# Kernel optimization log

Measured on AMD Instinct MI355X. Metric: run time of the kernel, lower is better.

The kernel has to match this reference:

```python
import jax, jax.numpy as jnp
import numpy as np

B, T, D = 2, 2048, 1024
DCD = 4096            # intermediate_dim
RET = 128             # expert_retrieval_dim (split into 2 halves of 64)
NEXP = 4096           # num experts (perfect square)
NKEYS = 64            # sqrt(NEXP)
H = 4                 # n_experts_heads
KPH = 8               # n_experts_per_head


def setup_inputs() -> dict:
    key = jax.random.key(0)
    ks = jax.random.split(key, 10)
    s = lambda k, shape, scale: jax.random.normal(k, shape, jnp.float32) * scale
    return {
        "hidden_states": jax.random.normal(ks[0], (B, T, D), jnp.float32),
        "Wg": s(ks[1], (D, DCD), 0.02), "bg": jnp.zeros((DCD,), jnp.float32),
        "Wu": s(ks[2], (D, DCD), 0.02), "bu": jnp.zeros((DCD,), jnp.float32),
        "Wd": s(ks[3], (DCD, D), 0.02), "bd": jnp.zeros((D,), jnp.float32),
        "Wq": s(ks[4], (D, RET * H), 0.02),          # queries proj (no bias)
        "keys": s(ks[5], (H, NKEYS, 2, RET // 2), 0.02),  # torch inits zeros; randn for a meaningful baseline
        "down_embed": s(ks[6], (NEXP, D), 0.02),
        "up_embed": s(ks[7], (NEXP, D), 0.02),
    }


def reference(hidden_states, Wg, bg, Wu, bu, Wd, bd, Wq, keys, down_embed, up_embed):
    b, t, d = hidden_states.shape
    # product-key retrieval: split query into two halves (p=2)
    q = (hidden_states @ Wq).reshape(b, t, 2, H, RET // 2)
    sim = jnp.einsum('btphn,hkpn->pbthk', q, keys)          # [2,b,t,H,NKEYS]
    sc, ix = jax.lax.top_k(sim, KPH)                        # per-half top-k
    sx, sy = sc[0], sc[1]
    ixx, ixy = ix[0], ix[1]
    all_sc = (sx[..., :, None] + sy[..., None, :]).reshape(b, t, H, KPH * KPH)
    all_ix = (ixx[..., :, None] * NKEYS + ixy[..., None, :]).reshape(b, t, H, KPH * KPH)
    scores, pk = jax.lax.top_k(all_sc, KPH)                 # [b,t,H,KPH]
    idx = jnp.take_along_axis(all_ix, pk, axis=-1)          # expert ids
    de = down_embed[idx]                                    # [b,t,H,KPH,D] gather
    ue = up_embed[idx]                                      # [b,t,H,KPH,D] gather
    w = jnp.einsum('btd,bthkd->bthk', hidden_states, de)
    w = jax.nn.silu(w) * jax.nn.softmax(scores, axis=-1)
    experts_states = jnp.einsum('bthk,bthkd->btd', w, ue)
    mlp = (jax.nn.silu(hidden_states @ Wg + bg) * (hidden_states @ Wu + bu)) @ Wd + bd
    return mlp + experts_states
```

## Files before the change

kernel.cpp:

```cpp
#include <hip/hip_runtime.h>
#include <hip/hip_bf16.h>
#include <stdint.h>

typedef unsigned short u16;
typedef __attribute__((ext_vector_type(8))) short short8;
typedef __attribute__((ext_vector_type(4))) float f32x4;
typedef __attribute__((ext_vector_type(2))) float f32x2;

union B8 { short8 v; u16 u[8]; };
union U4 { unsigned long long q; u16 u[4]; };

__device__ __forceinline__ float b2f(u16 b) {
  union { unsigned int i; float f; } x; x.i = ((unsigned int)b) << 16; return x.f;
}
__device__ __forceinline__ u16 f2b(float f) {
  __hip_bfloat16 h = __float2bfloat16(f);
  return *reinterpret_cast<u16*>(&h);
}

#define GLOAD_LDS16(gp, lp)                                                  \
  __builtin_amdgcn_global_load_lds(                                          \
      (const __attribute__((address_space(1))) unsigned int*)(gp),           \
      (__attribute__((address_space(3))) unsigned int*)(lp), 16, 0, 0)

__global__ __launch_bounds__(256) void cvt_f2b(const float* __restrict__ src,
                                               u16* __restrict__ dst) {
  size_t i = ((size_t)blockIdx.x * 256 + threadIdx.x) * 4;
  f32x4 v = *(const f32x4*)(src + i);
  U4 o;
#pragma unroll
  for (int j = 0; j < 4; ++j) o.u[j] = f2b(v[j]);
  *(unsigned long long*)(dst + i) = o.q;
}

__global__ __launch_bounds__(256) void convt_w(const float* __restrict__ W,
                                               u16* __restrict__ WT,
                                               int K, int N) {
  int k  = blockIdx.x * 64 + (threadIdx.x & 63);
  int n8 = blockIdx.y * 32 + (threadIdx.x >> 6) * 8;
  const float* p = W + (size_t)k * N + n8;
  f32x4 a = *(const f32x4*)(p);
  f32x4 b = *(const f32x4*)(p + 4);
#pragma unroll
  for (int j = 0; j < 4; ++j) WT[(size_t)(n8 + j) * K + k] = f2b(a[j]);
#pragma unroll
  for (int j = 0; j < 4; ++j) WT[(size_t)(n8 + 4 + j) * K + k] = f2b(b[j]);
}

__global__ __launch_bounds__(256) void convt_keys(const float* __restrict__ keys,
                                                  float* __restrict__ keysT) {
  int h = blockIdx.x, p = blockIdx.y;
  int k  = threadIdx.x >> 2;
  int n0 = (threadIdx.x & 3) * 16;
  const float* src = keys + ((size_t)(h * 64 + k) * 2 + p) * 64 + n0;
  float* dst = keysT + (((size_t)h * 2 + p) * 64) * 64 + k;
#pragma unroll
  for (int c = 0; c < 16; ++c)
    dst[(size_t)(n0 + c) * 64] = src[c];
}

__global__ __launch_bounds__(256) void gemm_bf16(
    const u16* __restrict__ A, const u16* __restrict__ BT,
    const float* __restrict__ bias,
    u16* __restrict__ Cb, int M, int N, int K)
{
  __shared__ __attribute__((aligned(16))) u16 As[128 * 64];
  __shared__ __attribute__((aligned(16))) u16 Bs[128 * 64];
  int tid = threadIdx.x;
  int m0 = blockIdx.y * 128, n0 = blockIdx.x * 128;
  int wave = tid >> 6, lane = tid & 63;
  int wm = (wave >> 1) * 64, wn = (wave & 1) * 64;
  int quad = lane >> 4, r16 = lane & 15;
  int s7 = r16 & 7;

  int srow = lane >> 3;
  int scol = ((lane & 7) ^ srow) * 8;
  const u16* aG = A  + (size_t)(m0 + wave * 32 + srow) * K + scol;
  const u16* bG = BT + (size_t)(n0 + wave * 32 + srow) * K + scol;

  f32x4 acc[4][4] = {};

  for (int k0 = 0; k0 < K; k0 += 64) {
#pragma unroll
    for (int idx = 0; idx < 4; ++idx) {
      size_t go = (size_t)idx * 8 * K + k0;
      int lo = wave * 2048 + idx * 512;
      GLOAD_LDS16(aG + go, As + lo);
      GLOAD_LDS16(bG + go, Bs + lo);
    }
    __syncthreads();
#pragma unroll
    for (int kk = 0; kk < 2; ++kk) {
      short8 af[4], bfr[4];
#pragma unroll
      for (int i = 0; i < 4; ++i)
        af[i] = *(const short8*)(&As[(wm + i * 16 + r16) * 64
                                     + (((kk << 2) + quad) ^ s7) * 8]);
#pragma unroll
      for (int j = 0; j < 4; ++j)
        bfr[j] = *(const short8*)(&Bs[(wn + j * 16 + r16) * 64
                                      + (((kk << 2) + quad) ^ s7) * 8]);
#pragma unroll
      for (int i = 0; i < 4; ++i)
#pragma unroll
        for (int j = 0; j < 4; ++j)
          acc[i][j] = __builtin_amdgcn_mfma_f32_16x16x32_bf16(af[i], bfr[j], acc[i][j], 0, 0, 0);
    }
    __syncthreads();
  }

#pragma unroll
  for (int i = 0; i < 4; ++i) {
    int row = m0 + wm + i * 16 + quad * 4;
#pragma unroll
    for (int j = 0; j < 4; ++j) {
      int col = n0 + wn + j * 16 + r16;
      float bv = bias ? bias[col] : 0.f;
#pragma unroll
      for (int r = 0; r < 4; ++r) {
        float v = acc[i][j][r] + bv;
        Cb[(size_t)(row + r) * N + col] = f2b(v);
      }
    }
  }
}

__global__ __launch_bounds__(256, 2) void gemm_gu(
    const u16* __restrict__ A, const u16* __restrict__ BgT,
    const u16* __restrict__ BuT,
    const float* __restrict__ bg, const float* __restrict__ bu,
    u16* __restrict__ H, int M, int N, int K)
{
  __shared__ __attribute__((aligned(16))) u16 As[128 * 64];
  __shared__ __attribute__((aligned(16))) u16 Gs[128 * 64];
  __shared__ __attribute__((aligned(16))) u16 Us[128 * 64];
  int tid = threadIdx.x;
  int m0 = blockIdx.y * 128, n0 = blockIdx.x * 128;
  int wave = tid >> 6, lane = tid & 63;
  int wm = (wave >> 1) * 64, wn = (wave & 1) * 64;
  int quad = lane >> 4, r16 = lane & 15;
  int s7 = r16 & 7;

  int srow = lane >> 3;
  int scol = ((lane & 7) ^ srow) * 8;
  const u16* aG = A   + (size_t)(m0 + wave * 32 + srow) * K + scol;
  const u16* gG = BgT + (size_t)(n0 + wave * 32 + srow) * K + scol;
  const u16* uG = BuT + (size_t)(n0 + wave * 32 + srow) * K + scol;

  f32x4 ag[4][4] = {}, au[4][4] = {};

  for (int k0 = 0; k0 < K; k0 += 64) {
#pragma unroll
    for (int idx = 0; idx < 4; ++idx) {
      size_t go = (size_t)idx * 8 * K + k0;
      int lo = wave * 2048 + idx * 512;
      GLOAD_LDS16(aG + go, As + lo);
      GLOAD_LDS16(gG + go, Gs + lo);
      GLOAD_LDS16(uG + go, Us + lo);
    }
    __syncthreads();
#pragma unroll
    for (int kk = 0; kk < 2; ++kk) {
      short8 af[4], bfr[4];
#pragma unroll
      for (int i = 0; i < 4; ++i)
        af[i] = *(const short8*)(&As[(wm + i * 16 + r16) * 64
                                     + (((kk << 2) + quad) ^ s7) * 8]);
#pragma unroll
      for (int j = 0; j < 4; ++j)
        bfr[j] = *(const short8*)(&Gs[(wn + j * 16 + r16) * 64
                                      + (((kk << 2) + quad) ^ s7) * 8]);
#pragma unroll
      for (int i = 0; i < 4; ++i)
#pragma unroll
        for (int j = 0; j < 4; ++j)
          ag[i][j] = __builtin_amdgcn_mfma_f32_16x16x32_bf16(af[i], bfr[j], ag[i][j], 0, 0, 0);
#pragma unroll
      for (int j = 0; j < 4; ++j)
        bfr[j] = *(const short8*)(&Us[(wn + j * 16 + r16) * 64
                                      + (((kk << 2) + quad) ^ s7) * 8]);
#pragma unroll
      for (int i = 0; i < 4; ++i)
#pragma unroll
        for (int j = 0; j < 4; ++j)
          au[i][j] = __builtin_amdgcn_mfma_f32_16x16x32_bf16(af[i], bfr[j], au[i][j], 0, 0, 0);
    }
    __syncthreads();
  }

#pragma unroll
  for (int i = 0; i < 4; ++i) {
    int row = m0 + wm + i * 16 + quad * 4;
#pragma unroll
    for (int j = 0; j < 4; ++j) {
      int col = n0 + wn + j * 16 + r16;
      float bgv = bg[col], buv = bu[col];
#pragma unroll
      for (int r = 0; r < 4; ++r) {
        float g = ag[i][j][r] + bgv;
        float u = au[i][j][r] + buv;
        float h = (g / (1.f + __expf(-g))) * u;
        H[(size_t)(row + r) * N + col] = f2b(h);
      }
    }
  }
}

__global__ __launch_bounds__(256) void gemm_dsk(
    const u16* __restrict__ A, const u16* __restrict__ BT,
    float* __restrict__ P, int M, int N, int K, int Kslice, int mOff)
{
  __shared__ __attribute__((aligned(16))) u16 As[128 * 64];
  __shared__ __attribute__((aligned(16))) u16 Bs[128 * 64];
  int tid = threadIdx.x;

  int lid = blockIdx.x + blockIdx.y * gridDim.x +
            blockIdx.z * gridDim.x * gridDim.y;
  int G = gridDim.y * gridDim.z;
  int n_blk, m_blk, z_blk;
  if ((G & 7) == 0) {
    int x = lid & 7, s = lid >> 3;
    int gid = x * (G >> 3) + (s >> 3);
    n_blk = s & 7;
    m_blk = gid % gridDim.y;
    z_blk = gid / gridDim.y;
  } else {
    n_blk = blockIdx.x; m_blk = blockIdx.y; z_blk = blockIdx.z;
  }

  int m0 = m_blk * 128, n0 = n_blk * 128;
  int kb = z_blk * Kslice, ke = kb + Kslice;
  int wave = tid >> 6, lane = tid & 63;
  int wm = (wave >> 1) * 64, wn = (wave & 1) * 64;
  int quad = lane >> 4, r16 = lane & 15;
  int s7 = r16 & 7;

  int srow = lane >> 3;
  int scol = ((lane & 7) ^ srow) * 8;
  const u16* aG = A  + (size_t)(m0 + wave * 32 + srow) * K + scol;
  const u16* bG = BT + (size_t)(n0 + wave * 32 + srow) * K + scol;

  f32x4 acc[4][4] = {};

  for (int k0 = kb; k0 < ke; k0 += 64) {
#pragma unroll
    for (int idx = 0; idx < 4; ++idx) {
      size_t go = (size_t)idx * 8 * K + k0;
      int lo = wave * 2048 + idx * 512;
      GLOAD_LDS16(aG + go, As + lo);
      GLOAD_LDS16(bG + go, Bs + lo);
    }
    __syncthreads();
#pragma unroll
    for (int kk = 0; kk < 2; ++kk) {
      short8 af[4], bfr[4];
#pragma unroll
      for (int i = 0; i < 4; ++i)
        af[i] = *(const short8*)(&As[(wm + i * 16 + r16) * 64
                                     + (((kk << 2) + quad) ^ s7) * 8]);
#pragma unroll
      for (int j = 0; j < 4; ++j)
        bfr[j] = *(const short8*)(&Bs[(wn + j * 16 + r16) * 64
                                      + (((kk << 2) + quad) ^ s7) * 8]);
#pragma unroll
      for (int i = 0; i < 4; ++i)
#pragma unroll
        for (int j = 0; j < 4; ++j)
          acc[i][j] = __builtin_amdgcn_mfma_f32_16x16x32_bf16(af[i], bfr[j], acc[i][j], 0, 0, 0);
    }
    __syncthreads();
  }

  float* Pz = P + (size_t)z_blk * 4194304;
#pragma unroll
  for (int i = 0; i < 4; ++i) {
    int row = mOff + m0 + wm + i * 16 + quad * 4;
#pragma unroll
    for (int j = 0; j < 4; ++j) {
      int col = n0 + wn + j * 16 + r16;
#pragma unroll
      for (int r = 0; r < 4; ++r)
        Pz[(size_t)(row + r) * N + col] = acc[i][j][r];
    }
  }
}

__global__ __launch_bounds__(256) void reduce_k(const float* __restrict__ part,
                                                int S,
                                                const float* __restrict__ es,
                                                const float* __restrict__ bd,
                                                float* __restrict__ out) {
  int t = blockIdx.x, c0 = threadIdx.x * 4;
  size_t off = (size_t)t * 1024 + c0;
  f32x4 a = *(const f32x4*)(es + off);
  for (int s = 0; s < S; ++s) {
    f32x4 p = *(const f32x4*)(part + (size_t)s * 4194304 + off);
#pragma unroll
    for (int c = 0; c < 4; ++c) a[c] += p[c];
  }
  f32x4 b = *(const f32x4*)(bd + c0);
  f32x4 o;
#pragma unroll
  for (int c = 0; c < 4; ++c) o[c] = a[c] + b[c];
  *(f32x4*)(out + off) = o;
}

template<int NP>
__device__ __forceinline__ void sort8_desc(float (&v)[NP], int (&ii)[NP], int j) {
#pragma unroll
  for (int k = 2; k <= 8; k <<= 1) {
#pragma unroll
    for (int s = k >> 1; s > 0; s >>= 1) {
      bool desc  = (j & k) == 0;
      bool lower = (j & s) == 0;
#pragma unroll
      for (int p = 0; p < NP; ++p) {
        float vp = __shfl_xor(v[p], s);
        int   ip = __shfl_xor(ii[p], s);
        bool mf = (v[p] > vp) || (v[p] == vp && ii[p] < ip);
        bool keep = (desc == lower) ? mf : !mf;
        if (!keep) { v[p] = vp; ii[p] = ip; }
      }
    }
  }
}

template<int NP>
__device__ __forceinline__ void merge_top8(float (&v)[NP], int (&ii)[NP], int j) {
#pragma unroll
  for (int r = 0; r < 3; ++r) {
    int mask = (8 << r) | 7;
#pragma unroll
    for (int p = 0; p < NP; ++p) {
      float vp = __shfl_xor(v[p], mask);
      int   ip = __shfl_xor(ii[p], mask);
      bool mf = (v[p] > vp) || (v[p] == vp && ii[p] < ip);
      if (!mf) { v[p] = vp; ii[p] = ip; }
    }
#pragma unroll
    for (int s = 4; s > 0; s >>= 1) {
      bool lower = (j & s) == 0;
#pragma unroll
      for (int p = 0; p < NP; ++p) {
        float vq = __shfl_xor(v[p], s);
        int   iq = __shfl_xor(ii[p], s);
        bool mf = (v[p] > vq) || (v[p] == vq && ii[p] < iq);
        bool keep = lower ? mf : !mf;
        if (!keep) { v[p] = vq; ii[p] = iq; }
      }
    }
  }
}

__global__ __launch_bounds__(256) void retrieve_k(
    const u16*  __restrict__ q,
    const float* __restrict__ keysT,
    int* __restrict__ idx_out,
    float* __restrict__ p_out)
{
  int t = blockIdx.x;
  int w = threadIdx.x >> 6, lane = threadIdx.x & 63;
  int j = lane & 7;

  float v[2]; int ii[2];
#pragma unroll
  for (int p = 0; p < 2; ++p) {
    const u16*   qp = q + (size_t)t * 512 + p * 256 + w * 64;
    const float* kp = keysT + ((size_t)(w * 2 + p) * 64) * 64 + lane;
    float s0 = 0.f, s1 = 0.f, s2 = 0.f, s3 = 0.f;
#pragma unroll
    for (int n = 0; n < 64; n += 8) {
      B8 qv; qv.v = *(const short8*)(qp + n);
      s0 += b2f(qv.u[0]) * kp[(size_t)(n + 0) * 64];
      s1 += b2f(qv.u[1]) * kp[(size_t)(n + 1) * 64];
      s2 += b2f(qv.u[2]) * kp[(size_t)(n + 2) * 64];
      s3 += b2f(qv.u[3]) * kp[(size_t)(n + 3) * 64];
      s0 += b2f(qv.u[4]) * kp[(size_t)(n + 4) * 64];
      s1 += b2f(qv.u[5]) * kp[(size_t)(n + 5) * 64];
      s2 += b2f(qv.u[6]) * kp[(size_t)(n + 6) * 64];
      s3 += b2f(qv.u[7]) * kp[(size_t)(n + 7) * 64];
    }
    v[p] = (s0 + s1) + (s2 + s3); ii[p] = lane;
  }

  sort8_desc<2>(v, ii, j);
  merge_top8<2>(v, ii, j);

  float v2[1] = { __shfl(v[0], lane >> 3) + __shfl(v[1], lane & 7) };
  int  pos[1] = { lane };
  merge_top8<1>(v2, pos, j);

  int ex = __shfl(ii[0], pos[0] >> 3);
  int ey = __shfl(ii[1], pos[0] & 7);

  float m = __shfl(v2[0], 0);
  float e = __expf(v2[0] - m);
  float sum = e;
#pragma unroll
  for (int s = 4; s > 0; s >>= 1) sum += __shfl_xor(sum, s);

  if (lane < 8) {
    int o = (t * 4 + w) * 8 + lane;
    p_out[o]   = e / sum;
    idx_out[o] = ex * 64 + ey;
  }
}

__global__ __launch_bounds__(512) void expert_k(
    const u16* __restrict__ xb, const u16* __restrict__ downb,
    const u16* __restrict__ upb,
    const int* __restrict__ idx, const float* __restrict__ probs,
    float* __restrict__ es)
{
  __shared__ float acc_s[8][1024];
  int t = blockIdx.x;
  int w = threadIdx.x >> 6, lane = threadIdx.x & 63;
  const size_t tb = (size_t)t * 1024;
  const int lo = lane * 8;

  B8 xv0, xv1;
  xv0.v = *(const short8*)(xb + tb + lo);
  xv1.v = *(const short8*)(xb + tb + 512 + lo);
  float xf[16];
#pragma unroll
  for (int c = 0; c < 8; ++c) { xf[c] = b2f(xv0.u[c]); xf[8 + c] = b2f(xv1.u[c]); }

  float a[16] = {};
#pragma unroll
  for (int e4 = 0; e4 < 4; ++e4) {
    int e = w * 4 + e4;
    int id = idx[t * 32 + e];
    const u16* dp = downb + (size_t)id * 1024;
    B8 d0, d1;
    d0.v = *(const short8*)(dp + lo);
    d1.v = *(const short8*)(dp + 512 + lo);
    float part = 0.f;
#pragma unroll
    for (int c = 0; c < 8; ++c)
      part += xf[c] * b2f(d0.u[c]) + xf[8 + c] * b2f(d1.u[c]);
#pragma unroll
    for (int off = 32; off; off >>= 1) part += __shfl_xor(part, off);
    float gate = (part / (1.f + __expf(-part))) * probs[t * 32 + e];
    const u16* upp = upb + (size_t)id * 1024;
    B8 u0, u1;
    u0.v = *(const short8*)(upp + lo);
    u1.v = *(const short8*)(upp + 512 + lo);
#pragma unroll
    for (int c = 0; c < 8; ++c) {
      a[c]     += gate * b2f(u0.u[c]);
      a[8 + c] += gate * b2f(u1.u[c]);
    }
  }
#pragma unroll
  for (int c = 0; c < 8; ++c) {
    acc_s[w][lo + c]       = a[c];
    acc_s[w][512 + lo + c] = a[8 + c];
  }
  __syncthreads();
  int d0i = threadIdx.x * 2;
  float o0 = 0.f, o1 = 0.f;
#pragma unroll
  for (int ww = 0; ww < 8; ++ww) {
    o0 += acc_s[ww][d0i];
    o1 += acc_s[ww][d0i + 1];
  }
  f32x2 o; o[0] = o0; o[1] = o1;
  *(f32x2*)(es + tb + d0i) = o;
}

extern "C" void kernel_launch(void* const* d_in, const int* in_sizes, int n_in,
                              void* d_out, int out_size, void* d_ws, size_t ws_size,
                              hipStream_t stream)
{
  const float* x    = (const float*)d_in[0];
  const float* Wg   = (const float*)d_in[1];
  const float* bg   = (const float*)d_in[2];
  const float* Wu   = (const float*)d_in[3];
  const float* bu   = (const float*)d_in[4];
  const float* Wd   = (const float*)d_in[5];
  const float* bd   = (const float*)d_in[6];
  const float* Wq   = (const float*)d_in[7];
  const float* keys = (const float*)d_in[8];
  const float* down = (const float*)d_in[9];
  const float* up   = (const float*)d_in[10];
  float* out = (float*)d_out;

  const size_t MB = 1048576;
  char* ws = (char*)d_ws;
  u16*   xb    = (u16*)(ws);
  u16*   WgT   = (u16*)(ws + 8  * MB);
  u16*   WuT   = (u16*)(ws + 16 * MB);
  u16*   WdT   = (u16*)(ws + 24 * MB);
  float* es    = (float*)(ws + 32 * MB);
  u16*   WqT   = (u16*)(ws + 32 * MB);
  u16*   qb    = (u16*)(ws + 34 * MB);
  float* keysT = (float*)(ws + 47 * MB);
  int*   idxb  = (int*)(ws + 48 * MB);
  float* prb   = (float*)(ws + 48 * MB + 512 * 1024);
  u16*   downb = (u16*)(ws + 49 * MB);
  u16*   upb   = (u16*)(ws + 57 * MB);

  int S = 2;
  while (S > 1 && 65 * MB + (size_t)S * 16 * MB + 1 * MB > ws_size) S >>= 1;
  float* part = (float*)(ws + 65 * MB);
  size_t gboff = 65 * MB + (size_t)S * 16 * MB;
  u16*   gb    = (u16*)(ws + gboff);

  size_t avail = ws_size > gboff ? ws_size - gboff : 0;
  int rows = 4096;
  while (rows > 128 && (size_t)rows * 4096 * 2 > avail) rows >>= 1;
  int Ksl = 4096 / S;

  cvt_f2b<<<4096, 256, 0, stream>>>(x, xb);
  cvt_f2b<<<4096, 256, 0, stream>>>(down, downb);
  cvt_f2b<<<4096, 256, 0, stream>>>(up, upb);
  convt_w<<<dim3(16, 16),  256, 0, stream>>>(Wq, WqT, 1024, 512);
  convt_w<<<dim3(16, 128), 256, 0, stream>>>(Wg, WgT, 1024, 4096);
  convt_w<<<dim3(16, 128), 256, 0, stream>>>(Wu, WuT, 1024, 4096);
  convt_w<<<dim3(64, 32),  256, 0, stream>>>(Wd, WdT, 4096, 1024);
  convt_keys<<<dim3(4, 2), 256, 0, stream>>>(keys, keysT);

  gemm_bf16<<<dim3(4, 32), 256, 0, stream>>>(xb, WqT, nullptr,
                                             qb, 4096, 512, 1024);
  retrieve_k<<<4096, 256, 0, stream>>>(qb, keysT, idxb, prb);
  expert_k<<<4096, 512, 0, stream>>>(xb, downb, upb, idxb, prb, es);

  for (int m0c = 0; m0c < 4096; m0c += rows) {
    int gy = rows / 128;
    gemm_gu<<<dim3(32, gy), 256, 0, stream>>>(xb + (size_t)m0c * 1024, WgT, WuT,
                                              bg, bu, gb, rows, 4096, 1024);
    gemm_dsk<<<dim3(8, gy, S), 256, 0, stream>>>(gb, WdT, part,
                                                 rows, 1024, 4096, Ksl, m0c);
  }
  reduce_k<<<4096, 256, 0, stream>>>(part, S, es, bd, out);
}
```

Before: 400.4 us.

## Enlarge gate/up GEMM tile, deepen K step, and merge conversion launches

The fused gate/up GEMM now uses 512-thread blocks computing 128x256 tiles with a K step of 128 and a new XOR swizzle for LDS. The down-projection split-K GEMM also moves to a K step of 128. The aim is more reuse per global load and fewer barriers per K. The three fp32-to-bf16 conversions become one launch, and the Wg/Wu transposes share one launch via blockIdx.z, to cut launch overhead. The trade-off is much more LDS per block: the gate/up kernel needs about 160KB, so at most one block fits per CU. That lowers occupancy and leaves no double buffering to hide memory latency.

```diff
diff --git a/kernel.cpp b/kernel.cpp
--- a/kernel.cpp
+++ b/kernel.cpp
@@ -23,9 +23,14 @@
       (const __attribute__((address_space(1))) unsigned int*)(gp),           \
       (__attribute__((address_space(3))) unsigned int*)(lp), 16, 0, 0)
 
-__global__ __launch_bounds__(256) void cvt_f2b(const float* __restrict__ src,
-                                               u16* __restrict__ dst) {
-  size_t i = ((size_t)blockIdx.x * 256 + threadIdx.x) * 4;
+__global__ __launch_bounds__(256) void cvt3(
+    const float* __restrict__ s0, const float* __restrict__ s1,
+    const float* __restrict__ s2,
+    u16* __restrict__ d0, u16* __restrict__ d1, u16* __restrict__ d2) {
+  int grp = blockIdx.x >> 12, blk = blockIdx.x & 4095;
+  const float* src = grp == 0 ? s0 : (grp == 1 ? s1 : s2);
+  u16*        dst = grp == 0 ? d0 : (grp == 1 ? d1 : d2);
+  size_t i = ((size_t)blk * 256 + threadIdx.x) * 4;
   f32x4 v = *(const f32x4*)(src + i);
   U4 o;
 #pragma unroll
@@ -33,9 +38,12 @@
   *(unsigned long long*)(dst + i) = o.q;
 }
 
-__global__ __launch_bounds__(256) void convt_w(const float* __restrict__ W,
-                                               u16* __restrict__ WT,
-                                               int K, int N) {
+__global__ __launch_bounds__(256) void convt_w(
+    const float* __restrict__ W0, u16* __restrict__ WT0,
+    const float* __restrict__ W1, u16* __restrict__ WT1,
+    int K, int N) {
+  const float* W = blockIdx.z ? W1 : W0;
+  u16* WT = blockIdx.z ? WT1 : WT0;
   int k  = blockIdx.x * 64 + (threadIdx.x & 63);
   int n8 = blockIdx.y * 32 + (threadIdx.x >> 6) * 8;
   const float* p = W + (size_t)k * N + n8;
@@ -125,51 +133,49 @@
   }
 }
 
-__global__ __launch_bounds__(256, 2) void gemm_gu(
+__global__ __launch_bounds__(512, 2) void gemm_gu(
     const u16* __restrict__ A, const u16* __restrict__ BgT,
     const u16* __restrict__ BuT,
     const float* __restrict__ bg, const float* __restrict__ bu,
     u16* __restrict__ H, int M, int N, int K)
 {
-  __shared__ __attribute__((aligned(16))) u16 As[128 * 64];
-  __shared__ __attribute__((aligned(16))) u16 Gs[128 * 64];
-  __shared__ __attribute__((aligned(16))) u16 Us[128 * 64];
+  __shared__ __attribute__((aligned(16))) u16 As[128 * 128];
+  __shared__ __attribute__((aligned(16))) u16 Gs[256 * 128];
+  __shared__ __attribute__((aligned(16))) u16 Us[256 * 128];
   int tid = threadIdx.x;
-  int m0 = blockIdx.y * 128, n0 = blockIdx.x * 128;
-  int wave = tid >> 6, lane = tid & 63;
-  int wm = (wave >> 1) * 64, wn = (wave & 1) * 64;
+  int m0 = blockIdx.y * 128, n0 = blockIdx.x * 256;
+  int wid = tid >> 6, lane = tid & 63;
+  int wm2 = (wid >> 2) * 64, wn2 = (wid & 3) * 64;
   int quad = lane >> 4, r16 = lane & 15;
-  int s7 = r16 & 7;
-
-  int srow = lane >> 3;
-  int scol = ((lane & 7) ^ srow) * 8;
-  const u16* aG = A   + (size_t)(m0 + wave * 32 + srow) * K + scol;
-  const u16* gG = BgT + (size_t)(n0 + wave * 32 + srow) * K + scol;
-  const u16* uG = BuT + (size_t)(n0 + wave * 32 + srow) * K + scol;
+  int r4 = lane >> 4;
+  int cblk = ((lane & 15) ^ (r4 << 2)) * 8;
+
+  const u16* aG = A   + (size_t)(m0 + wid * 16 + r4) * K + cblk;
+  const u16* gG = BgT + (size_t)(n0 + wid * 32 + r4) * K + cblk;
+  const u16* uG = BuT + (size_t)(n0 + wid * 32 + r4) * K + cblk;
 
   f32x4 ag[4][4] = {}, au[4][4] = {};
 
-  for (int k0 = 0; k0 < K; k0 += 64) {
-#pragma unroll
-    for (int idx = 0; idx < 4; ++idx) {
-      size_t go = (size_t)idx * 8 * K + k0;
-      int lo = wave * 2048 + idx * 512;
-      GLOAD_LDS16(aG + go, As + lo);
-      GLOAD_LDS16(gG + go, Gs + lo);
-      GLOAD_LDS16(uG + go, Us + lo);
+  for (int k0 = 0; k0 < K; k0 += 128) {
+#pragma unroll
+    for (int idx = 0; idx < 4; ++idx)
+      GLOAD_LDS16(aG + (size_t)idx * 4 * K + k0, As + (wid * 16 + idx * 4) * 128);
+#pragma unroll
+    for (int idx = 0; idx < 8; ++idx) {
+      GLOAD_LDS16(gG + (size_t)idx * 4 * K + k0, Gs + (wid * 32 + idx * 4) * 128);
+      GLOAD_LDS16(uG + (size_t)idx * 4 * K + k0, Us + (wid * 32 + idx * 4) * 128);
     }
     __syncthreads();
 #pragma unroll
-    for (int kk = 0; kk < 2; ++kk) {
+    for (int kk = 0; kk < 4; ++kk) {
+      int cb = ((((kk << 2) + quad) ^ ((r16 & 3) << 2))) * 8;
       short8 af[4], bfr[4];
 #pragma unroll
       for (int i = 0; i < 4; ++i)
-        af[i] = *(const short8*)(&As[(wm + i * 16 + r16) * 64
-                                     + (((kk << 2) + quad) ^ s7) * 8]);
+        af[i] = *(const short8*)(&As[(wm2 + i * 16 + r16) * 128 + cb]);
 #pragma unroll
       for (int j = 0; j < 4; ++j)
-        bfr[j] = *(const short8*)(&Gs[(wn + j * 16 + r16) * 64
-                                      + (((kk << 2) + quad) ^ s7) * 8]);
+        bfr[j] = *(const short8*)(&Gs[(wn2 + j * 16 + r16) * 128 + cb]);
 #pragma unroll
       for (int i = 0; i < 4; ++i)
 #pragma unroll
@@ -177,8 +183,7 @@
           ag[i][j] = __builtin_amdgcn_mfma_f32_16x16x32_bf16(af[i], bfr[j], ag[i][j], 0, 0, 0);
 #pragma unroll
       for (int j = 0; j < 4; ++j)
-        bfr[j] = *(const short8*)(&Us[(wn + j * 16 + r16) * 64
-                                      + (((kk << 2) + quad) ^ s7) * 8]);
+        bfr[j] = *(const short8*)(&Us[(wn2 + j * 16 + r16) * 128 + cb]);
 #pragma unroll
       for (int i = 0; i < 4; ++i)
 #pragma unroll
@@ -190,10 +195,10 @@
 
 #pragma unroll
   for (int i = 0; i < 4; ++i) {
-    int row = m0 + wm + i * 16 + quad * 4;
+    int row = m0 + wm2 + i * 16 + quad * 4;
 #pragma unroll
     for (int j = 0; j < 4; ++j) {
-      int col = n0 + wn + j * 16 + r16;
+      int col = n0 + wn2 + j * 16 + r16;
       float bgv = bg[col], buv = bu[col];
 #pragma unroll
       for (int r = 0; r < 4; ++r) {
@@ -210,8 +215,8 @@
     const u16* __restrict__ A, const u16* __restrict__ BT,
     float* __restrict__ P, int M, int N, int K, int Kslice, int mOff)
 {
-  __shared__ __attribute__((aligned(16))) u16 As[128 * 64];
-  __shared__ __attribute__((aligned(16))) u16 Bs[128 * 64];
+  __shared__ __attribute__((aligned(16))) u16 As[128 * 128];
+  __shared__ __attribute__((aligned(16))) u16 Bs[128 * 128];
   int tid = threadIdx.x;
 
   int lid = blockIdx.x + blockIdx.y * gridDim.x +
@@ -233,35 +238,33 @@
   int wave = tid >> 6, lane = tid & 63;
   int wm = (wave >> 1) * 64, wn = (wave & 1) * 64;
   int quad = lane >> 4, r16 = lane & 15;
-  int s7 = r16 & 7;
-
-  int srow = lane >> 3;
-  int scol = ((lane & 7) ^ srow) * 8;
-  const u16* aG = A  + (size_t)(m0 + wave * 32 + srow) * K + scol;
-  const u16* bG = BT + (size_t)(n0 + wave * 32 + srow) * K + scol;
+  int r4 = lane >> 4;
+  int cblk = ((lane & 15) ^ (r4 << 2)) * 8;
+
+  const u16* aG = A  + (size_t)(m0 + wave * 32 + r4) * K + cblk;
+  const u16* bG = BT + (size_t)(n0 + wave * 32 + r4) * K + cblk;
 
   f32x4 acc[4][4] = {};
 
-  for (int k0 = kb; k0 < ke; k0 += 64) {
-#pragma unroll
-    for (int idx = 0; idx < 4; ++idx) {
-      size_t go = (size_t)idx * 8 * K + k0;
-      int lo = wave * 2048 + idx * 512;
+  for (int k0 = kb; k0 < ke; k0 += 128) {
+#pragma unroll
+    for (int idx = 0; idx < 8; ++idx) {
+      size_t go = (size_t)idx * 4 * K + k0;
+      int lo = (wave * 32 + idx * 4) * 128;
       GLOAD_LDS16(aG + go, As + lo);
       GLOAD_LDS16(bG + go, Bs + lo);
     }
     __syncthreads();
 #pragma unroll
-    for (int kk = 0; kk < 2; ++kk) {
+    for (int kk = 0; kk < 4; ++kk) {
+      int cb = ((((kk << 2) + quad) ^ ((r16 & 3) << 2))) * 8;
       short8 af[4], bfr[4];
 #pragma unroll
       for (int i = 0; i < 4; ++i)
-        af[i] = *(const short8*)(&As[(wm + i * 16 + r16) * 64
-                                     + (((kk << 2) + quad) ^ s7) * 8]);
+        af[i] = *(const short8*)(&As[(wm + i * 16 + r16) * 128 + cb]);
 #pragma unroll
       for (int j = 0; j < 4; ++j)
-        bfr[j] = *(const short8*)(&Bs[(wn + j * 16 + r16) * 64
-                                      + (((kk << 2) + quad) ^ s7) * 8]);
+        bfr[j] = *(const short8*)(&Bs[(wn + j * 16 + r16) * 128 + cb]);
 #pragma unroll
       for (int i = 0; i < 4; ++i)
 #pragma unroll
@@ -511,13 +514,10 @@
   while (rows > 128 && (size_t)rows * 4096 * 2 > avail) rows >>= 1;
   int Ksl = 4096 / S;
 
-  cvt_f2b<<<4096, 256, 0, stream>>>(x, xb);
-  cvt_f2b<<<4096, 256, 0, stream>>>(down, downb);
-  cvt_f2b<<<4096, 256, 0, stream>>>(up, upb);
-  convt_w<<<dim3(16, 16),  256, 0, stream>>>(Wq, WqT, 1024, 512);
-  convt_w<<<dim3(16, 128), 256, 0, stream>>>(Wg, WgT, 1024, 4096);
-  convt_w<<<dim3(16, 128), 256, 0, stream>>>(Wu, WuT, 1024, 4096);
-  convt_w<<<dim3(64, 32),  256, 0, stream>>>(Wd, WdT, 4096, 1024);
+  cvt3<<<12288, 256, 0, stream>>>(x, down, up, xb, downb, upb);
+  convt_w<<<dim3(16, 16),  256, 0, stream>>>(Wq, WqT, nullptr, nullptr, 1024, 512);
+  convt_w<<<dim3(16, 128, 2), 256, 0, stream>>>(Wg, WgT, Wu, WuT, 1024, 4096);
+  convt_w<<<dim3(64, 32),  256, 0, stream>>>(Wd, WdT, nullptr, nullptr, 4096, 1024);
   convt_keys<<<dim3(4, 2), 256, 0, stream>>>(keys, keysT);
 
   gemm_bf16<<<dim3(4, 32), 256, 0, stream>>>(xb, WqT, nullptr,
@@ -527,7 +527,7 @@
 
   for (int m0c = 0; m0c < 4096; m0c += rows) {
     int gy = rows / 128;
-    gemm_gu<<<dim3(32, gy), 256, 0, stream>>>(xb + (size_t)m0c * 1024, WgT, WuT,
+    gemm_gu<<<dim3(16, gy), 512, 0, stream>>>(xb + (size_t)m0c * 1024, WgT, WuT,
                                               bg, bu, gb, rows, 4096, 1024);
     gemm_dsk<<<dim3(8, gy, S), 256, 0, stream>>>(gb, WdT, part,
                                                  rows, 1024, 4096, Ksl, m0c);
```

Measured after the change: 406.6 us. About the same (+1.6%).

## Double K-tile depth in down-proj GEMM and merge conversion kernel launches

Applied to the files above, without the earlier changes.

The down-projection split-K GEMM now stages 128-wide K tiles in LDS instead of 64, using a new XOR swizzle for the wider rows. This halves the number of barrier pairs per K loop and gives more MFMA work per sync, at the cost of doubling LDS use to 64KB per block, which may lower occupancy. Separately, the three fp32-to-bf16 conversions are fused into one launch, and the Wg/Wu transposes share one launch through the z grid dimension, to cut launch overhead.

```diff
diff --git a/kernel.cpp b/kernel.cpp
--- a/kernel.cpp
+++ b/kernel.cpp
@@ -23,9 +23,14 @@
       (const __attribute__((address_space(1))) unsigned int*)(gp),           \
       (__attribute__((address_space(3))) unsigned int*)(lp), 16, 0, 0)
 
-__global__ __launch_bounds__(256) void cvt_f2b(const float* __restrict__ src,
-                                               u16* __restrict__ dst) {
-  size_t i = ((size_t)blockIdx.x * 256 + threadIdx.x) * 4;
+__global__ __launch_bounds__(256) void cvt3(
+    const float* __restrict__ s0, const float* __restrict__ s1,
+    const float* __restrict__ s2,
+    u16* __restrict__ d0, u16* __restrict__ d1, u16* __restrict__ d2) {
+  int grp = blockIdx.x >> 12, blk = blockIdx.x & 4095;
+  const float* src = grp == 0 ? s0 : (grp == 1 ? s1 : s2);
+  u16*        dst = grp == 0 ? d0 : (grp == 1 ? d1 : d2);
+  size_t i = ((size_t)blk * 256 + threadIdx.x) * 4;
   f32x4 v = *(const f32x4*)(src + i);
   U4 o;
 #pragma unroll
@@ -33,9 +38,12 @@
   *(unsigned long long*)(dst + i) = o.q;
 }
 
-__global__ __launch_bounds__(256) void convt_w(const float* __restrict__ W,
-                                               u16* __restrict__ WT,
-                                               int K, int N) {
+__global__ __launch_bounds__(256) void convt_w(
+    const float* __restrict__ W0, u16* __restrict__ WT0,
+    const float* __restrict__ W1, u16* __restrict__ WT1,
+    int K, int N) {
+  const float* W = blockIdx.z ? W1 : W0;
+  u16* WT = blockIdx.z ? WT1 : WT0;
   int k  = blockIdx.x * 64 + (threadIdx.x & 63);
   int n8 = blockIdx.y * 32 + (threadIdx.x >> 6) * 8;
   const float* p = W + (size_t)k * N + n8;
@@ -210,8 +218,8 @@
     const u16* __restrict__ A, const u16* __restrict__ BT,
     float* __restrict__ P, int M, int N, int K, int Kslice, int mOff)
 {
-  __shared__ __attribute__((aligned(16))) u16 As[128 * 64];
-  __shared__ __attribute__((aligned(16))) u16 Bs[128 * 64];
+  __shared__ __attribute__((aligned(16))) u16 As[128 * 128];
+  __shared__ __attribute__((aligned(16))) u16 Bs[128 * 128];
   int tid = threadIdx.x;
 
   int lid = blockIdx.x + blockIdx.y * gridDim.x +
@@ -233,35 +241,34 @@
   int wave = tid >> 6, lane = tid & 63;
   int wm = (wave >> 1) * 64, wn = (wave & 1) * 64;
   int quad = lane >> 4, r16 = lane & 15;
-  int s7 = r16 & 7;
-
-  int srow = lane >> 3;
-  int scol = ((lane & 7) ^ srow) * 8;
-  const u16* aG = A  + (size_t)(m0 + wave * 32 + srow) * K + scol;
-  const u16* bG = BT + (size_t)(n0 + wave * 32 + srow) * K + scol;
+  int r4 = lane >> 4;
+  int c  = lane & 15;
+
+  const u16* aBase = A  + (size_t)(m0 + wave * 32 + r4) * K;
+  const u16* bBase = BT + (size_t)(n0 + wave * 32 + r4) * K;
 
   f32x4 acc[4][4] = {};
 
-  for (int k0 = kb; k0 < ke; k0 += 64) {
-#pragma unroll
-    for (int idx = 0; idx < 4; ++idx) {
-      size_t go = (size_t)idx * 8 * K + k0;
-      int lo = wave * 2048 + idx * 512;
-      GLOAD_LDS16(aG + go, As + lo);
-      GLOAD_LDS16(bG + go, Bs + lo);
+  for (int k0 = kb; k0 < ke; k0 += 128) {
+#pragma unroll
+    for (int idx = 0; idx < 8; ++idx) {
+      int sc = (c ^ r4 ^ ((idx & 1) << 2)) * 8;
+      size_t go = (size_t)idx * 4 * K + k0 + sc;
+      int lo = (wave * 32 + idx * 4) * 128;
+      GLOAD_LDS16(aBase + go, As + lo);
+      GLOAD_LDS16(bBase + go, Bs + lo);
     }
     __syncthreads();
 #pragma unroll
-    for (int kk = 0; kk < 2; ++kk) {
+    for (int kk = 0; kk < 4; ++kk) {
+      int cb = (((kk << 2) + quad) ^ (r16 & 7)) * 8;
       short8 af[4], bfr[4];
 #pragma unroll
       for (int i = 0; i < 4; ++i)
-        af[i] = *(const short8*)(&As[(wm + i * 16 + r16) * 64
-                                     + (((kk << 2) + quad) ^ s7) * 8]);
+        af[i] = *(const short8*)(&As[(wm + i * 16 + r16) * 128 + cb]);
 #pragma unroll
       for (int j = 0; j < 4; ++j)
-        bfr[j] = *(const short8*)(&Bs[(wn + j * 16 + r16) * 64
-                                      + (((kk << 2) + quad) ^ s7) * 8]);
+        bfr[j] = *(const short8*)(&Bs[(wn + j * 16 + r16) * 128 + cb]);
 #pragma unroll
       for (int i = 0; i < 4; ++i)
 #pragma unroll
@@ -511,13 +518,10 @@
   while (rows > 128 && (size_t)rows * 4096 * 2 > avail) rows >>= 1;
   int Ksl = 4096 / S;
 
-  cvt_f2b<<<4096, 256, 0, stream>>>(x, xb);
-  cvt_f2b<<<4096, 256, 0, stream>>>(down, downb);
-  cvt_f2b<<<4096, 256, 0, stream>>>(up, upb);
-  convt_w<<<dim3(16, 16),  256, 0, stream>>>(Wq, WqT, 1024, 512);
-  convt_w<<<dim3(16, 128), 256, 0, stream>>>(Wg, WgT, 1024, 4096);
-  convt_w<<<dim3(16, 128), 256, 0, stream>>>(Wu, WuT, 1024, 4096);
-  convt_w<<<dim3(64, 32),  256, 0, stream>>>(Wd, WdT, 4096, 1024);
+  cvt3<<<12288, 256, 0, stream>>>(x, down, up, xb, downb, upb);
+  convt_w<<<dim3(16, 16),  256, 0, stream>>>(Wq, WqT, nullptr, nullptr, 1024, 512);
+  convt_w<<<dim3(16, 128, 2), 256, 0, stream>>>(Wg, WgT, Wu, WuT, 1024, 4096);
+  convt_w<<<dim3(64, 32),  256, 0, stream>>>(Wd, WdT, nullptr, nullptr, 4096, 1024);
   convt_keys<<<dim3(4, 2), 256, 0, stream>>>(keys, keysT);
 
   gemm_bf16<<<dim3(4, 32), 256, 0, stream>>>(xb, WqT, nullptr,
```

New measurement: 398.0 us. No clear change (-0.6%).
